# Optimization experiments

Hardware: AMD Instinct MI355X
Metric: run time of the kernel (lower is better)

Reference implementation:

```python
import jax, jax.numpy as jnp
import numpy as np

N = 1048576   # total items across all bags
F = 64        # num_features
C = 128       # out_channel
B = 4096      # number of bags (batch)


def setup_inputs() -> dict:
    key = jax.random.key(0)
    k1, k2, k3 = jax.random.split(key, 3)
    x = jax.random.normal(k1, (N, F), dtype=jnp.float32)
    w = jax.random.normal(k2, (F, C), dtype=jnp.float32) * (1.0 / np.sqrt(F))
    segment_ids = jnp.sort(jax.random.randint(k3, (N,), 0, B, dtype=jnp.int32))
    return {"x": x, "w": w, "segment_ids": segment_ids, "num_segments": B}


def reference(x, w, segment_ids, num_segments):
    # Per-item: sigmoid(x_i @ W) in [C]; per-bag: sum of per-item results.
    s = jax.nn.sigmoid(x @ w)                                  # [N, C]
    out = jax.ops.segment_sum(s, segment_ids,
                              num_segments=num_segments)        # [B, C]
    return out
```

## Files before the change

### kernel.cpp

```cpp
#include <hip/hip_runtime.h>
#include <hip/hip_bf16.h>

#define F 64
#define C 128
#define SPAN 128
#define NT (SPAN / 16)

typedef __attribute__((ext_vector_type(8))) short short8;
typedef __attribute__((ext_vector_type(4))) float floatx4;

__device__ __forceinline__ unsigned short f32_to_bf16_rne(float f) {
    unsigned int u = __builtin_bit_cast(unsigned int, f);
    unsigned int r = u + 0x7FFFu + ((u >> 16) & 1u);
    return (unsigned short)(r >> 16);
}

__device__ __forceinline__ short bf16c(float f) {
    return __builtin_bit_cast(short, __float2bfloat16(f));
}

__device__ __forceinline__ float fast_sigmoid(float v) {
    float e = __builtin_amdgcn_exp2f(v * -1.44269504088896f);
    return __builtin_amdgcn_rcpf(1.0f + e);
}

__global__ __launch_bounds__(256) void prep_kernel(
    const float* __restrict__ w, float* __restrict__ out,
    unsigned short* __restrict__ wsfrag, int out_f4)
{
    const int b = blockIdx.x;
    if (b < (int)gridDim.x - 1) {
        int idx = b * 256 + threadIdx.x;
        if (idx < out_f4) ((float4*)out)[idx] = make_float4(0.f, 0.f, 0.f, 0.f);
    } else {
        #pragma unroll
        for (int i = 0; i < 4; ++i) {
            int idx = threadIdx.x * 4 + i;
            int lane = idx & 63;
            int ks   = (idx >> 6) & 1;
            int nf   = idx >> 7;
            int col  = nf * 16 + (lane & 15);
            int kg   = (lane >> 4) * 8;
            unsigned short* dst = wsfrag + (size_t)idx * 8;
            #pragma unroll
            for (int e = 0; e < 8; ++e) {
                int k = ks * 32 + kg + e;
                dst[e] = f32_to_bf16_rne(w[k * C + col]);
            }
        }
    }
}

__global__ __launch_bounds__(256, 3) void fused_seg_gemm(
    const float* __restrict__ x, const unsigned short* __restrict__ wsfrag,
    const int* __restrict__ seg, float* __restrict__ out)
{
    const int tid  = threadIdx.x;
    const int lane = tid & 63;
    const int wave = tid >> 6;
    const int l15  = lane & 15;
    const int g    = lane >> 4;
    const long long base = ((long long)blockIdx.x * 4 + wave) * SPAN;

    short8 bfrag[8][2];
    {
        const short8* fb = (const short8*)wsfrag;
        #pragma unroll
        for (int nf = 0; nf < 8; ++nf)
            #pragma unroll
            for (int ks = 0; ks < 2; ++ks)
                bfrag[nf][ks] = fb[(nf * 2 + ks) * 64 + lane];
    }

    const float4* xp = (const float4*)(x + base * F);
    const int fi = l15 * 16 + g * 2;

    float4 c0 = xp[fi], c1 = xp[fi + 1], c2 = xp[fi + 8], c3 = xp[fi + 9];
    int s = seg[base + l15];

    float runsum[8];
    #pragma unroll
    for (int nf = 0; nf < 8; ++nf) runsum[nf] = 0.0f;
    int cur_seg = -1;

    auto flush = [&]() {
        if (cur_seg >= 0) {
            #pragma unroll
            for (int nf = 0; nf < 8; ++nf) {
                float v = runsum[nf];
                v += __shfl_xor(v, 16);
                v += __shfl_xor(v, 32);
                if (lane < 16) atomicAdd(&out[cur_seg * C + nf * 16 + lane], v);
                runsum[nf] = 0.0f;
            }
        }
        cur_seg = -1;
    };

    #pragma unroll 2
    for (int t = 0; t < NT; ++t) {
        float4 n0, n1, n2, n3; int ns = s;
        const bool more = (t + 1 < NT);
        if (more) {
            int nfi = fi + (t + 1) * 256;
            n0 = xp[nfi]; n1 = xp[nfi + 1]; n2 = xp[nfi + 8]; n3 = xp[nfi + 9];
            ns = seg[base + (t + 1) * 16 + l15];
        }

        short8 a0, a1;
        a0[0] = bf16c(c0.x); a0[1] = bf16c(c0.y); a0[2] = bf16c(c0.z); a0[3] = bf16c(c0.w);
        a0[4] = bf16c(c1.x); a0[5] = bf16c(c1.y); a0[6] = bf16c(c1.z); a0[7] = bf16c(c1.w);
        a1[0] = bf16c(c2.x); a1[1] = bf16c(c2.y); a1[2] = bf16c(c2.z); a1[3] = bf16c(c2.w);
        a1[4] = bf16c(c3.x); a1[5] = bf16c(c3.y); a1[6] = bf16c(c3.z); a1[7] = bf16c(c3.w);

        floatx4 acc[8];
        #pragma unroll
        for (int nf = 0; nf < 8; ++nf) {
            acc[nf] = (floatx4)0.0f;
            acc[nf] = __builtin_amdgcn_mfma_f32_16x16x32_bf16(a0, bfrag[nf][0], acc[nf], 0, 0, 0);
            acc[nf] = __builtin_amdgcn_mfma_f32_16x16x32_bf16(a1, bfrag[nf][1], acc[nf], 0, 0, 0);
        }

        const int u0 = __shfl(s, 0), u15 = __shfl(s, 15);
        if (u0 == u15) {
            if (u0 != cur_seg) { flush(); cur_seg = u0; }
            #pragma unroll
            for (int nf = 0; nf < 8; ++nf)
                #pragma unroll
                for (int r = 0; r < 4; ++r)
                    runsum[nf] += fast_sigmoid(acc[nf][r]);
        } else {
            flush();
            const int sr0 = __shfl(s, g * 4 + 0), sr1 = __shfl(s, g * 4 + 1);
            const int sr2 = __shfl(s, g * 4 + 2), sr3 = __shfl(s, g * 4 + 3);
            #pragma unroll
            for (int nf = 0; nf < 8; ++nf) {
                const int col = nf * 16 + l15;
                float run = fast_sigmoid(acc[nf][0]);
                int   rs  = sr0;
                float v;
                v = fast_sigmoid(acc[nf][1]);
                if (sr1 != rs) { atomicAdd(&out[rs * C + col], run); rs = sr1; run = v; } else run += v;
                v = fast_sigmoid(acc[nf][2]);
                if (sr2 != rs) { atomicAdd(&out[rs * C + col], run); rs = sr2; run = v; } else run += v;
                v = fast_sigmoid(acc[nf][3]);
                if (sr3 != rs) { atomicAdd(&out[rs * C + col], run); rs = sr3; run = v; } else run += v;
                atomicAdd(&out[rs * C + col], run);
            }
        }

        if (more) { c0 = n0; c1 = n1; c2 = n2; c3 = n3; s = ns; }
    }
    flush();
}

extern "C" void kernel_launch(void* const* d_in, const int* in_sizes, int n_in,
                              void* d_out, int out_size, void* d_ws, size_t ws_size,
                              hipStream_t stream) {
    const float* x  = (const float*)d_in[0];
    const float* w  = (const float*)d_in[1];
    const int* seg  = (const int*)d_in[2];
    float* out      = (float*)d_out;

    const int n = in_sizes[0] / F;
    const int nblocks = n / (4 * SPAN);

    const int out_f4 = out_size / 4;
    const int zblocks = (out_f4 + 255) / 256;

    prep_kernel<<<zblocks + 1, 256, 0, stream>>>(
        w, out, (unsigned short*)d_ws, out_f4);

    fused_seg_gemm<<<nblocks, 256, 0, stream>>>(
        x, (const unsigned short*)d_ws, seg, out);
}
```

Before: 63.86 us.

## Stage weights in LDS, double-buffer x loads two tiles ahead, batch segment-id loads

Weight fragments now go into shared memory instead of 64 VGPRs per lane, and occupancy rises from 3 to 4 blocks per CU. The x tile loop is fully unrolled with two register buffers, so loads are issued two tiles ahead. All 128 segment ids for a wave are read up front in two coalesced loads and picked out with shuffles. The aim is more memory-level parallelism and hidden latency for this bandwidth-bound kernel. The cost is an LDS read per MFMA and a block-wide barrier at start.

```diff
diff --git a/kernel.cpp b/kernel.cpp
--- a/kernel.cpp
+++ b/kernel.cpp
@@ -51,10 +51,12 @@
     }
 }
 
-__global__ __launch_bounds__(256, 3) void fused_seg_gemm(
+__global__ __launch_bounds__(256, 4) void fused_seg_gemm(
     const float* __restrict__ x, const unsigned short* __restrict__ wsfrag,
     const int* __restrict__ seg, float* __restrict__ out)
 {
+    __shared__ unsigned short wlds[16 * 64 * 8];
+
     const int tid  = threadIdx.x;
     const int lane = tid & 63;
     const int wave = tid >> 6;
@@ -62,21 +64,18 @@
     const int g    = lane >> 4;
     const long long base = ((long long)blockIdx.x * 4 + wave) * SPAN;
 
-    short8 bfrag[8][2];
     {
         const short8* fb = (const short8*)wsfrag;
+        short8* fl = (short8*)wlds;
         #pragma unroll
-        for (int nf = 0; nf < 8; ++nf)
-            #pragma unroll
-            for (int ks = 0; ks < 2; ++ks)
-                bfrag[nf][ks] = fb[(nf * 2 + ks) * 64 + lane];
+        for (int i = 0; i < 4; ++i) fl[tid + i * 256] = fb[tid + i * 256];
     }
+
+    int sg0 = seg[base + lane];
+    int sg1 = seg[base + 64 + lane];
 
     const float4* xp = (const float4*)(x + base * F);
     const int fi = l15 * 16 + g * 2;
-
-    float4 c0 = xp[fi], c1 = xp[fi + 1], c2 = xp[fi + 8], c3 = xp[fi + 9];
-    int s = seg[base + l15];
 
     float runsum[8];
     #pragma unroll
@@ -97,31 +96,36 @@
         cur_seg = -1;
     };
 
-    #pragma unroll 2
-    for (int t = 0; t < NT; ++t) {
-        float4 n0, n1, n2, n3; int ns = s;
-        const bool more = (t + 1 < NT);
-        if (more) {
-            int nfi = fi + (t + 1) * 256;
-            n0 = xp[nfi]; n1 = xp[nfi + 1]; n2 = xp[nfi + 8]; n3 = xp[nfi + 9];
-            ns = seg[base + (t + 1) * 16 + l15];
-        }
+    float4 bufA[4], bufB[4];
+    #define ISSUE(B, T) { const int o = fi + (T) * 256; \
+        B[0] = xp[o]; B[1] = xp[o + 1]; B[2] = xp[o + 8]; B[3] = xp[o + 9]; }
 
+    ISSUE(bufA, 0);
+    ISSUE(bufB, 1);
+    __syncthreads();
+
+    auto step = [&](float4* buf, int t) {
         short8 a0, a1;
-        a0[0] = bf16c(c0.x); a0[1] = bf16c(c0.y); a0[2] = bf16c(c0.z); a0[3] = bf16c(c0.w);
-        a0[4] = bf16c(c1.x); a0[5] = bf16c(c1.y); a0[6] = bf16c(c1.z); a0[7] = bf16c(c1.w);
-        a1[0] = bf16c(c2.x); a1[1] = bf16c(c2.y); a1[2] = bf16c(c2.z); a1[3] = bf16c(c2.w);
-        a1[4] = bf16c(c3.x); a1[5] = bf16c(c3.y); a1[6] = bf16c(c3.z); a1[7] = bf16c(c3.w);
+        a0[0] = bf16c(buf[0].x); a0[1] = bf16c(buf[0].y); a0[2] = bf16c(buf[0].z); a0[3] = bf16c(buf[0].w);
+        a0[4] = bf16c(buf[1].x); a0[5] = bf16c(buf[1].y); a0[6] = bf16c(buf[1].z); a0[7] = bf16c(buf[1].w);
+        a1[0] = bf16c(buf[2].x); a1[1] = bf16c(buf[2].y); a1[2] = bf16c(buf[2].z); a1[3] = bf16c(buf[2].w);
+        a1[4] = bf16c(buf[3].x); a1[5] = bf16c(buf[3].y); a1[6] = bf16c(buf[3].z); a1[7] = bf16c(buf[3].w);
+        if (t + 2 < NT) ISSUE(buf, t + 2);
 
+        const short8* bl = (const short8*)wlds;
         floatx4 acc[8];
         #pragma unroll
         for (int nf = 0; nf < 8; ++nf) {
+            short8 b0 = bl[(nf * 2 + 0) * 64 + lane];
+            short8 b1 = bl[(nf * 2 + 1) * 64 + lane];
             acc[nf] = (floatx4)0.0f;
-            acc[nf] = __builtin_amdgcn_mfma_f32_16x16x32_bf16(a0, bfrag[nf][0], acc[nf], 0, 0, 0);
-            acc[nf] = __builtin_amdgcn_mfma_f32_16x16x32_bf16(a1, bfrag[nf][1], acc[nf], 0, 0, 0);
+            acc[nf] = __builtin_amdgcn_mfma_f32_16x16x32_bf16(a0, b0, acc[nf], 0, 0, 0);
+            acc[nf] = __builtin_amdgcn_mfma_f32_16x16x32_bf16(a1, b1, acc[nf], 0, 0, 0);
         }
 
-        const int u0 = __shfl(s, 0), u15 = __shfl(s, 15);
+        const int sreg = (t < 4) ? sg0 : sg1;
+        const int tb   = (t & 3) * 16;
+        const int u0 = __shfl(sreg, tb), u15 = __shfl(sreg, tb + 15);
         if (u0 == u15) {
             if (u0 != cur_seg) { flush(); cur_seg = u0; }
             #pragma unroll
@@ -131,8 +135,8 @@
                     runsum[nf] += fast_sigmoid(acc[nf][r]);
         } else {
             flush();
-            const int sr0 = __shfl(s, g * 4 + 0), sr1 = __shfl(s, g * 4 + 1);
-            const int sr2 = __shfl(s, g * 4 + 2), sr3 = __shfl(s, g * 4 + 3);
+            const int sr0 = __shfl(sreg, tb + g * 4 + 0), sr1 = __shfl(sreg, tb + g * 4 + 1);
+            const int sr2 = __shfl(sreg, tb + g * 4 + 2), sr3 = __shfl(sreg, tb + g * 4 + 3);
             #pragma unroll
             for (int nf = 0; nf < 8; ++nf) {
                 const int col = nf * 16 + l15;
@@ -148,10 +152,12 @@
                 atomicAdd(&out[rs * C + col], run);
             }
         }
+    };
 
-        if (more) { c0 = n0; c1 = n1; c2 = n2; c3 = n3; s = ns; }
-    }
+    step(bufA, 0); step(bufB, 1); step(bufA, 2); step(bufB, 3);
+    step(bufA, 4); step(bufB, 5); step(bufA, 6); step(bufB, 7);
     flush();
+    #undef ISSUE
 }
 
 extern "C" void kernel_launch(void* const* d_in, const int* in_sizes, int n_in,
```

New measurement: 131.0 us. 105% more time.
